# Performance work log

Measured on AMD Instinct MI355X. Metric: run time of the kernel, lower is better.

The kernel has to match this reference:

```python
import jax, jax.numpy as jnp
import numpy as np

N = 50000          # nodes
E = 1_600_000      # directed edges (before self loops)
G = 128            # graphs in batch
IN_F = 64
C1, H = 32, 4      # gat1: out_channels=32, heads=4 -> hidden 128
C2 = 64            # gat2: out_channels=64, heads=1, concat=False
OUT_F = 2
EPS = 1e-5
NEG_SLOPE = 0.2    # PyG GATv2Conv default


def setup_inputs() -> dict:
    key = jax.random.key(0)
    ks = jax.random.split(key, 24)
    s = 0.05
    inp = {
        'x': jax.random.normal(ks[0], (N, IN_F), jnp.float32),
        'edge_index': jax.random.randint(ks[1], (2, E), 0, N, dtype=jnp.int64),
        'batch': jnp.sort(jax.random.randint(ks[2], (N,), 0, G, dtype=jnp.int64)),
        # GATv2 layer 1 (in=64 -> 4 heads x 32)
        'W1l': jax.random.normal(ks[3], (IN_F, H * C1), jnp.float32) * s,
        'b1l': jnp.zeros((H * C1,), jnp.float32),
        'W1r': jax.random.normal(ks[4], (IN_F, H * C1), jnp.float32) * s,
        'b1r': jnp.zeros((H * C1,), jnp.float32),
        'att1': jax.random.normal(ks[5], (H, C1), jnp.float32) * s,
        'bias1': jnp.zeros((H * C1,), jnp.float32),
        # GATv2 layer 2 (in=128 -> 1 head x 64, no concat)
        'W2l': jax.random.normal(ks[6], (H * C1, C2), jnp.float32) * s,
        'b2l': jnp.zeros((C2,), jnp.float32),
        'W2r': jax.random.normal(ks[7], (H * C1, C2), jnp.float32) * s,
        'b2r': jnp.zeros((C2,), jnp.float32),
        'att2': jax.random.normal(ks[8], (1, C2), jnp.float32) * s,
        'bias2': jnp.zeros((C2,), jnp.float32),
        # batchnorms (batch-statistics normalization)
        'bn1_g': jnp.ones((H * C1,), jnp.float32),
        'bn1_b': jnp.zeros((H * C1,), jnp.float32),
        'bn2_g': jnp.ones((C2,), jnp.float32),
        'bn2_b': jnp.zeros((C2,), jnp.float32),
        # final linear: CL2_F*3 -> out_f
        'lin_w': jax.random.normal(ks[9], (3 * C2, OUT_F), jnp.float32) * s,
        'lin_b': jnp.zeros((OUT_F,), jnp.float32),
    }
    return inp


def _gatv2(x, Wl, bl, Wr, br, att, bias, src, dst, heads, ch, concat, n_nodes):
    # x: [N, F_in]; src/dst: [E'] (self loops already appended)
    xl = (x @ Wl + bl).reshape(n_nodes, heads, ch)  # source transform
    xr = (x @ Wr + br).reshape(n_nodes, heads, ch)  # target transform
    m = jax.nn.leaky_relu(xl[src] + xr[dst], NEG_SLOPE)      # [E', H, C]
    logits = jnp.einsum('ehc,hc->eh', m, att)                # [E', H]
    # segment softmax over destination nodes (every node has a self loop)
    mx = jax.ops.segment_max(logits, dst, num_segments=n_nodes)
    a = jnp.exp(logits - mx[dst])
    denom = jax.ops.segment_sum(a, dst, num_segments=n_nodes)
    alpha = a / denom[dst]                                   # [E', H]
    out = jax.ops.segment_sum(xl[src] * alpha[..., None], dst,
                              num_segments=n_nodes)          # [N, H, C]
    if concat:
        out = out.reshape(n_nodes, heads * ch)
    else:
        out = out.mean(axis=1)
    return out + bias


def _bn(h, gamma, beta):
    mu = h.mean(axis=0)
    var = h.var(axis=0)
    return (h - mu) * jax.lax.rsqrt(var + EPS) * gamma + beta


def reference(x, edge_index, batch, W1l, b1l, W1r, b1r, att1, bias1,
              W2l, b2l, W2r, b2r, att2, bias2,
              bn1_g, bn1_b, bn2_g, bn2_b, lin_w, lin_b):
    n = x.shape[0]
    loops = jnp.arange(n, dtype=edge_index.dtype)
    src = jnp.concatenate([edge_index[0], loops])  # PyG add_self_loops=True
    dst = jnp.concatenate([edge_index[1], loops])

    h = jax.nn.relu(_gatv2(x, W1l, b1l, W1r, b1r, att1, bias1,
                           src, dst, H, C1, True, n))
    h = _bn(h, bn1_g, bn1_b)      # dropout is identity (eval)
    h = jax.nn.relu(_gatv2(h, W2l, b2l, W2r, b2r, att2, bias2,
                           src, dst, 1, C2, False, n))
    h = _bn(h, bn2_g, bn2_b)

    x0 = jax.ops.segment_sum(h, batch, num_segments=G)                  # add pool
    cnt = jax.ops.segment_sum(jnp.ones((n, 1), h.dtype), batch, num_segments=G)
    x1 = x0 / jnp.maximum(cnt, 1.0)                                     # mean pool
    x2 = jax.ops.segment_max(h, batch, num_segments=G)                  # max pool
    feat = jnp.concatenate([x0, x1, x2], axis=-1)                       # [G, 3*C2]
    return feat @ lin_w + lin_b
```

## Files before the change

### kernel.cpp

```cpp
#include <hip/hip_runtime.h>
#include <hip/hip_fp16.h>
#include <math.h>

#define BSHIFT 7
#define CHUNK  8192
#define CAP    6144

__device__ inline __half2 habs2_(__half2 x){
  union { __half2 h; unsigned u; } c; c.h = x; c.u &= 0x7FFF7FFFu; return c.h;
}
__device__ inline __half2 lrelu2_(__half2 x, __half2 c06, __half2 c04){
  return __hfma2(c04, habs2_(x), __hmul2(c06, x));
}

__global__ __launch_bounds__(256) void k_pre(const int* __restrict__ ei, int E, int N, int NB,
    int* __restrict__ bfill, unsigned* __restrict__ ebuf,
    const float* __restrict__ X,
    const float* __restrict__ Wl, const float* __restrict__ bl,
    const float* __restrict__ Wr, const float* __restrict__ br,
    __half* __restrict__ outl, __half* __restrict__ outr, int bb){
  __shared__ float xs[32][64];
  if ((int)blockIdx.x < bb){
    int* hist = (int*)&xs[0][0];
    int base = blockIdx.x*CHUNK;
    int EL = E + N;
    int end = min(base + CHUNK, EL);
    for (int i = threadIdx.x; i < NB; i += 256) hist[i] = 0;
    __syncthreads();
    for (int e = base + threadIdx.x; e < end; e += 256){
      int d = (e < E) ? ei[E + e] : (e - E);
      atomicAdd(&hist[d >> BSHIFT], 1);
    }
    __syncthreads();
    for (int b = threadIdx.x; b < NB; b += 256){
      int c = hist[b];
      hist[b] = (c > 0) ? (b*CAP + atomicAdd(&bfill[b], c)) : 0;
    }
    __syncthreads();
    for (int e = base + threadIdx.x; e < end; e += 256){
      int s, d;
      if (e < E){ s = ei[e]; d = ei[E + e]; } else { s = d = e - E; }
      int pos = atomicAdd(&hist[d >> BSHIFT], 1);
      ebuf[pos] = (unsigned)s | ((unsigned)d << 16);
    }
  } else {
    const int tid = threadIdx.x;
    const int n0 = ((int)blockIdx.x - bb)*32;
    for (int t = tid; t < 32*64; t += 256){
      int r = t >> 6, c = t & 63;
      int node = n0 + r;
      xs[r][c] = (node < N) ? X[(size_t)node*64 + c] : 0.f;
    }
    __syncthreads();
    const int jg = tid & 63;
    const int ng = tid >> 6;
    const int q  = jg*4;
    const bool isL = (q < 128);
    const float* W = isL ? Wl : Wr;
    const int jj   = isL ? q : q - 128;
    const float* bbp = isL ? bl : br;
    __half* OUT    = isL ? outl : outr;
    const float4 bias4 = *(const float4*)(bbp + jj);
    float acc[8][4];
    #pragma unroll
    for (int n = 0; n < 8; ++n){ acc[n][0]=acc[n][1]=acc[n][2]=acc[n][3]=0.f; }
    for (int k = 0; k < 64; k += 4){
      const float4 w0 = *(const float4*)(W + (size_t)(k+0)*128 + jj);
      const float4 w1 = *(const float4*)(W + (size_t)(k+1)*128 + jj);
      const float4 w2 = *(const float4*)(W + (size_t)(k+2)*128 + jj);
      const float4 w3 = *(const float4*)(W + (size_t)(k+3)*128 + jj);
      #pragma unroll
      for (int n = 0; n < 8; ++n){
        const float4 xv = *(const float4*)(&xs[ng*8 + n][k]);
        acc[n][0] = fmaf(xv.w,w3.x, fmaf(xv.z,w2.x, fmaf(xv.y,w1.x, fmaf(xv.x,w0.x, acc[n][0]))));
        acc[n][1] = fmaf(xv.w,w3.y, fmaf(xv.z,w2.y, fmaf(xv.y,w1.y, fmaf(xv.x,w0.y, acc[n][1]))));
        acc[n][2] = fmaf(xv.w,w3.z, fmaf(xv.z,w2.z, fmaf(xv.y,w1.z, fmaf(xv.x,w0.z, acc[n][2]))));
        acc[n][3] = fmaf(xv.w,w3.w, fmaf(xv.z,w2.w, fmaf(xv.y,w1.w, fmaf(xv.x,w0.w, acc[n][3]))));
      }
    }
    #pragma unroll
    for (int n = 0; n < 8; ++n){
      int node = n0 + ng*8 + n;
      if (node < N){
        union { __half2 h[2]; uint2 u; } cv;
        cv.h[0] = __floats2half2_rn(acc[n][0]+bias4.x, acc[n][1]+bias4.y);
        cv.h[1] = __floats2half2_rn(acc[n][2]+bias4.z, acc[n][3]+bias4.w);
        *(uint2*)(OUT + (size_t)node*128 + jj) = cv.u;
      }
    }
  }
}

__global__ __launch_bounds__(1024) void k_fine(const unsigned* __restrict__ ebuf,
    const int* __restrict__ bfill, int N, int NB,
    int* __restrict__ rstart, int* __restrict__ rend, int* __restrict__ esrc){
  __shared__ int cnt[128];
  __shared__ int sc[128];
  __shared__ int base[128];
  int b = blockIdx.x;
  int n0 = b << BSHIFT;
  int nn = min(128, N - n0);
  int e0 = b*CAP;
  int e1 = e0 + bfill[b];
  if (threadIdx.x < 128) cnt[threadIdx.x] = 0;
  __syncthreads();
  for (int e = e0 + threadIdx.x; e < e1; e += 1024)
    atomicAdd(&cnt[(ebuf[e] >> 16) & 127], 1);
  __syncthreads();
  if (threadIdx.x < 128) sc[threadIdx.x] = cnt[threadIdx.x];
  __syncthreads();
  for (int off = 1; off < 128; off <<= 1){
    int v = 0;
    if (threadIdx.x < 128 && (int)threadIdx.x >= off) v = sc[threadIdx.x - off];
    __syncthreads();
    if (threadIdx.x < 128) sc[threadIdx.x] += v;
    __syncthreads();
  }
  if (threadIdx.x < 128){
    int bs = e0 + sc[threadIdx.x] - cnt[threadIdx.x];
    base[threadIdx.x] = bs;
    if ((int)threadIdx.x < nn){
      rstart[n0 + threadIdx.x] = bs;
      rend[n0 + threadIdx.x]   = bs + cnt[threadIdx.x];
    }
    cnt[threadIdx.x] = 0;
  }
  __syncthreads();
  for (int e = e0 + threadIdx.x; e < e1; e += 1024){
    unsigned pk = ebuf[e];
    int local = (int)(pk >> 16) & 127;
    int pos = base[local] + atomicAdd(&cnt[local], 1);
    esrc[pos] = (int)(pk & 0xffffu);
  }
}

__global__ __launch_bounds__(256) void k_dhist(const int* __restrict__ rstart, const int* __restrict__ rend,
                                               int N, int* __restrict__ dh){
  __shared__ int h[512];
  for (int i = threadIdx.x; i < 512; i += 256) h[i] = 0;
  __syncthreads();
  #pragma unroll
  for (int k = 0; k < 4; ++k){
    int n = blockIdx.x*1024 + k*256 + threadIdx.x;
    if (n < N){
      int deg = rend[n] - rstart[n];
      atomicAdd(&h[511 - min(deg, 511)], 1);
    }
  }
  __syncthreads();
  for (int i = threadIdx.x; i < 512; i += 256){
    int c = h[i];
    if (c) atomicAdd(&dh[i], c);
  }
}

__global__ __launch_bounds__(512) void k_dscan(const int* __restrict__ dh, int* __restrict__ dfill){
  __shared__ int s[512];
  int tid = threadIdx.x;
  int v = dh[tid];
  s[tid] = v; __syncthreads();
  for (int off = 1; off < 512; off <<= 1){
    int t = (tid >= off) ? s[tid - off] : 0;
    __syncthreads();
    s[tid] += t;
    __syncthreads();
  }
  dfill[tid] = s[tid] - v;
}

__global__ __launch_bounds__(256) void k_dperm(const int* __restrict__ rstart, const int* __restrict__ rend,
                                               int N, int* __restrict__ dfill, int* __restrict__ perm){
  __shared__ int h[512];
  __shared__ int mybin[1024];
  int base_n = blockIdx.x*1024;
  for (int i = threadIdx.x; i < 512; i += 256) h[i] = 0;
  __syncthreads();
  #pragma unroll
  for (int k = 0; k < 4; ++k){
    int n = base_n + k*256 + threadIdx.x;
    if (n < N){
      int deg = rend[n] - rstart[n];
      int b = 511 - min(deg, 511);
      mybin[k*256 + threadIdx.x] = b;
      atomicAdd(&h[b], 1);
    }
  }
  __syncthreads();
  for (int i = threadIdx.x; i < 512; i += 256){
    int c = h[i];
    h[i] = c ? atomicAdd(&dfill[i], c) : 0;
  }
  __syncthreads();
  #pragma unroll
  for (int k = 0; k < 4; ++k){
    int n = base_n + k*256 + threadIdx.x;
    if (n < N){
      int pos = atomicAdd(&h[mybin[k*256 + threadIdx.x]], 1);
      perm[pos] = n;
    }
  }
}

__global__ __launch_bounds__(256) void k_gemm2(const __half2* __restrict__ X2,
    const float* __restrict__ Wl, const float* __restrict__ bl,
    const float* __restrict__ Wr, const float* __restrict__ br,
    __half* __restrict__ outl, __half* __restrict__ outr, int N,
    const float* __restrict__ bsum, const float* __restrict__ bsq,
    const float* __restrict__ gam, const float* __restrict__ bet){
  __shared__ float xs[32][128];
  const int tid = threadIdx.x;
  const int n0 = blockIdx.x*32;
  const float invN = 1.f/(float)N;
  for (int t = tid; t < 32*64; t += 256){
    int r = t >> 6, c2 = t & 63, c = c2*2;
    int node = n0 + r;
    float2 v = (node < N) ? __half22float2(X2[(size_t)node*64 + c2]) : make_float2(0.f,0.f);
    float m0 = bsum[c]*invN,   m1 = bsum[c+1]*invN;
    float r0 = rsqrtf(bsq[c]*invN   - m0*m0 + 1e-5f);
    float r1 = rsqrtf(bsq[c+1]*invN - m1*m1 + 1e-5f);
    v.x = (v.x - m0) * r0 * gam[c  ] + bet[c  ];
    v.y = (v.y - m1) * r1 * gam[c+1] + bet[c+1];
    xs[r][c] = v.x; xs[r][c+1] = v.y;
  }
  __syncthreads();
  const int jg = tid & 31;
  const int ng = tid >> 5;
  const int q  = jg*4;
  const bool isL = (q < 64);
  const float* W = isL ? Wl : Wr;
  const int jj   = isL ? q : q - 64;
  const float* bbp = isL ? bl : br;
  __half* OUT    = isL ? outl : outr;
  const float4 bias4 = *(const float4*)(bbp + jj);
  float acc[4][4];
  #pragma unroll
  for (int n = 0; n < 4; ++n){ acc[n][0]=acc[n][1]=acc[n][2]=acc[n][3]=0.f; }
  for (int k = 0; k < 128; k += 4){
    const float4 w0 = *(const float4*)(W + (size_t)(k+0)*64 + jj);
    const float4 w1 = *(const float4*)(W + (size_t)(k+1)*64 + jj);
    const float4 w2 = *(const float4*)(W + (size_t)(k+2)*64 + jj);
    const float4 w3 = *(const float4*)(W + (size_t)(k+3)*64 + jj);
    #pragma unroll
    for (int n = 0; n < 4; ++n){
      const float4 xv = *(const float4*)(&xs[ng*4 + n][k]);
      acc[n][0] = fmaf(xv.w,w3.x, fmaf(xv.z,w2.x, fmaf(xv.y,w1.x, fmaf(xv.x,w0.x, acc[n][0]))));
      acc[n][1] = fmaf(xv.w,w3.y, fmaf(xv.z,w2.y, fmaf(xv.y,w1.y, fmaf(xv.x,w0.y, acc[n][1]))));
      acc[n][2] = fmaf(xv.w,w3.z, fmaf(xv.z,w2.z, fmaf(xv.y,w1.z, fmaf(xv.x,w0.z, acc[n][2]))));
      acc[n][3] = fmaf(xv.w,w3.w, fmaf(xv.z,w2.w, fmaf(xv.y,w1.w, fmaf(xv.x,w0.w, acc[n][3]))));
    }
  }
  #pragma unroll
  for (int n = 0; n < 4; ++n){
    int node = n0 + ng*4 + n;
    if (node < N){
      union { __half2 h[2]; uint2 u; } cv;
      cv.h[0] = __floats2half2_rn(acc[n][0]+bias4.x, acc[n][1]+bias4.y);
      cv.h[1] = __floats2half2_rn(acc[n][2]+bias4.z, acc[n][3]+bias4.w);
      *(uint2*)(OUT + (size_t)node*64 + jj) = cv.u;
    }
  }
}

__global__ __launch_bounds__(256, 6) void k_gat1(const __half* __restrict__ xl, const __half* __restrict__ xr,
    const int* __restrict__ rstart, const int* __restrict__ rend,
    const int* __restrict__ esrc, const int* __restrict__ perm,
    const float* __restrict__ att, const float* __restrict__ bias,
    __half* __restrict__ h1, int N){
  int wv = (blockIdx.x*256 + threadIdx.x) >> 6;
  int lane = threadIdx.x & 63;
  int g = lane >> 4;
  int t = lane & 15;
  int idx = wv*4 + g;
  bool live = idx < N;
  int nd = perm[min(idx, N-1)];
  int c0 = t*8;
  const __half2 c06 = __float2half2_rn(0.6f);
  const __half2 c04 = __float2half2_rn(0.4f);
  union { uint4 u; __half2 h[4]; } xru;
  xru.u = *(const uint4*)(xr + (size_t)nd*128 + c0);
  float4 a0 = *(const float4*)(att + c0);
  float4 a1 = *(const float4*)(att + c0 + 4);
  __half2 av2[4] = { __floats2half2_rn(a0.x,a0.y), __floats2half2_rn(a0.z,a0.w),
                     __floats2half2_rn(a1.x,a1.y), __floats2half2_rn(a1.z,a1.w) };
  int r0 = rstart[nd];
  int r1 = rend[nd];
  int d  = r1 - r0;
  d = max(d, __shfl_xor(d, 16));
  d = max(d, __shfl_xor(d, 32));
  const char* xb = (const char*)xl;
  const unsigned cb = (unsigned)(c0*2);
  float s = 0.f;
  __half2 acc2[4];
  #pragma unroll
  for (int k = 0; k < 4; ++k) acc2[k] = __float2half2_rn(0.f);
  union V { uint4 u; __half2 h[4]; } cur[4], nxt[4];
  #pragma unroll
  for (int q = 0; q < 4; ++q){
    unsigned j = (unsigned)esrc[r0 + q] & 0xFFFFu;
    cur[q].u = *(const uint4*)(xb + ((j << 8) + cb));
  }
  for (int i = 0; i < d; i += 4){
    #pragma unroll
    for (int q = 0; q < 4; ++q){
      unsigned j = (unsigned)esrc[r0 + i + 4 + q] & 0xFFFFu;
      nxt[q].u = *(const uint4*)(xb + ((j << 8) + cb));
    }
    #pragma unroll
    for (int q = 0; q < 4; ++q){
      bool valid = (r0 + i + q) < r1;
      __half2 p2 = __float2half2_rn(0.f);
      #pragma unroll
      for (int k = 0; k < 4; ++k){
        __half2 m2 = __hadd2(cur[q].h[k], xru.h[k]);
        p2 = __hfma2(lrelu2_(m2, c06, c04), av2[k], p2);
      }
      float p = __low2float(p2) + __high2float(p2);
      p += __shfl_xor(p, 1);
      p += __shfl_xor(p, 2);
      float w = valid ? __expf(p) : 0.f;
      s += w;
      __half2 w2 = __float2half2_rn(w);
      #pragma unroll
      for (int k = 0; k < 4; ++k) acc2[k] = __hfma2(w2, cur[q].h[k], acc2[k]);
    }
    #pragma unroll
    for (int q = 0; q < 4; ++q) cur[q] = nxt[q];
  }
  if (live){
    float inv = 1.f/s;
    float4 b0 = *(const float4*)(bias + c0);
    float4 b1 = *(const float4*)(bias + c0 + 4);
    float bv[8] = {b0.x,b0.y,b0.z,b0.w,b1.x,b1.y,b1.z,b1.w};
    union { __half2 h[4]; uint4 u; } o;
    #pragma unroll
    for (int k = 0; k < 4; ++k){
      float2 af = __half22float2(acc2[k]);
      float f0 = fmaxf(af.x*inv + bv[2*k],   0.f);
      float f1 = fmaxf(af.y*inv + bv[2*k+1], 0.f);
      o.h[k] = __floats2half2_rn(f0, f1);
    }
    *(uint4*)(h1 + (size_t)nd*128 + c0) = o.u;
  }
}

__global__ __launch_bounds__(256, 6) void k_gat2(const __half* __restrict__ xl, const __half* __restrict__ xr,
    const int* __restrict__ rstart, const int* __restrict__ rend,
    const int* __restrict__ esrc, const int* __restrict__ perm,
    const float* __restrict__ att, const float* __restrict__ bias,
    __half* __restrict__ h2, int N){
  int wv = (blockIdx.x*256 + threadIdx.x) >> 6;
  int lane = threadIdx.x & 63;
  int g = lane >> 3;
  int t = lane & 7;
  int idx = wv*8 + g;
  bool live = idx < N;
  int nd = perm[min(idx, N-1)];
  int c0 = t*8;
  const __half2 c06 = __float2half2_rn(0.6f);
  const __half2 c04 = __float2half2_rn(0.4f);
  union { uint4 u; __half2 h[4]; } xru;
  xru.u = *(const uint4*)(xr + (size_t)nd*64 + c0);
  float4 a0 = *(const float4*)(att + c0);
  float4 a1 = *(const float4*)(att + c0 + 4);
  __half2 av2[4] = { __floats2half2_rn(a0.x,a0.y), __floats2half2_rn(a0.z,a0.w),
                     __floats2half2_rn(a1.x,a1.y), __floats2half2_rn(a1.z,a1.w) };
  int r0 = rstart[nd];
  int r1 = rend[nd];
  int d  = r1 - r0;
  d = max(d, __shfl_xor(d, 8));
  d = max(d, __shfl_xor(d, 16));
  d = max(d, __shfl_xor(d, 32));
  const char* xb = (const char*)xl;
  const unsigned cb = (unsigned)(c0*2);
  float s = 0.f;
  __half2 acc2[4];
  #pragma unroll
  for (int k = 0; k < 4; ++k) acc2[k] = __float2half2_rn(0.f);
  union V { uint4 u; __half2 h[4]; } cur[4], nxt[4];
  #pragma unroll
  for (int q = 0; q < 4; ++q){
    unsigned j = (unsigned)esrc[r0 + q] & 0xFFFFu;
    cur[q].u = *(const uint4*)(xb + ((j << 7) + cb));
  }
  for (int i = 0; i < d; i += 4){
    #pragma unroll
    for (int q = 0; q < 4; ++q){
      unsigned j = (unsigned)esrc[r0 + i + 4 + q] & 0xFFFFu;
      nxt[q].u = *(const uint4*)(xb + ((j << 7) + cb));
    }
    #pragma unroll
    for (int q = 0; q < 4; ++q){
      bool valid = (r0 + i + q) < r1;
      __half2 p2 = __float2half2_rn(0.f);
      #pragma unroll
      for (int k = 0; k < 4; ++k){
        __half2 m2 = __hadd2(cur[q].h[k], xru.h[k]);
        p2 = __hfma2(lrelu2_(m2, c06, c04), av2[k], p2);
      }
      float p = __low2float(p2) + __high2float(p2);
      p += __shfl_xor(p, 1);
      p += __shfl_xor(p, 2);
      p += __shfl_xor(p, 4);
      float w = valid ? __expf(p) : 0.f;
      s += w;
      __half2 w2 = __float2half2_rn(w);
      #pragma unroll
      for (int k = 0; k < 4; ++k) acc2[k] = __hfma2(w2, cur[q].h[k], acc2[k]);
    }
    #pragma unroll
    for (int q = 0; q < 4; ++q) cur[q] = nxt[q];
  }
  if (live){
    float inv = 1.f/s;
    float4 b0 = *(const float4*)(bias + c0);
    float4 b1 = *(const float4*)(bias + c0 + 4);
    float bv[8] = {b0.x,b0.y,b0.z,b0.w,b1.x,b1.y,b1.z,b1.w};
    union { __half2 h[4]; uint4 u; } o;
    #pragma unroll
    for (int k = 0; k < 4; ++k){
      float2 af = __half22float2(acc2[k]);
      float f0 = fmaxf(af.x*inv + bv[2*k],   0.f);
      float f1 = fmaxf(af.y*inv + bv[2*k+1], 0.f);
      o.h[k] = __floats2half2_rn(f0, f1);
    }
    *(uint4*)(h2 + (size_t)nd*64 + c0) = o.u;
  }
}

template<int C>
__global__ __launch_bounds__(256) void k_bnstats(const __half* __restrict__ h, int N,
    float* __restrict__ sum, float* __restrict__ sq){
  constexpr int RPB = 256/C;
  int c = threadIdx.x % C;
  int sub = threadIdx.x / C;
  float s = 0.f, q = 0.f;
  for (int r = blockIdx.x*RPB + sub; r < N; r += gridDim.x*RPB){
    float v = __half2float(h[(size_t)r*C + c]);
    s += v; q += v*v;
  }
  __shared__ float ls[256], lq[256];
  ls[threadIdx.x] = s; lq[threadIdx.x] = q;
  __syncthreads();
  if (threadIdx.x < C){
    float S = ls[c], Q = lq[c];
    #pragma unroll
    for (int u = 1; u < RPB; ++u){ S += ls[u*C + c]; Q += lq[u*C + c]; }
    atomicAdd(&sum[c], S);
    atomicAdd(&sq[c], Q);
  }
}

__global__ __launch_bounds__(256) void k_pool(const __half* __restrict__ h2, const int* __restrict__ batch, int N,
    const float* __restrict__ bsum, const float* __restrict__ bsq,
    const float* __restrict__ g, const float* __restrict__ b,
    const float* __restrict__ lw, const float* __restrict__ lb,
    float* __restrict__ out){
  int gr = blockIdx.x;
  int lo = 0, hi = N;
  while (lo < hi){ int mid = (lo+hi)>>1; if (batch[mid] < gr) lo = mid+1; else hi = mid; }
  int r0 = lo;
  lo = r0; hi = N;
  while (lo < hi){ int mid = (lo+hi)>>1; if (batch[mid] < gr+1) lo = mid+1; else hi = mid; }
  int r1 = lo;
  int c = threadIdx.x & 63;
  int sub = threadIdx.x >> 6;
  const float invN = 1.f/(float)N;
  float m = bsum[c]*invN;
  float rs = rsqrtf(bsq[c]*invN - m*m + 1e-5f);
  float aff_s = rs*g[c];
  float aff_b = b[c] - m*aff_s;
  float s = 0.f, mx = -INFINITY;
  for (int r = r0 + sub; r < r1; r += 4){
    float v = __half2float(h2[(size_t)r*64 + c])*aff_s + aff_b;
    s += v; mx = fmaxf(mx, v);
  }
  __shared__ float ls[256], lm[256], ft[192];
  ls[threadIdx.x] = s; lm[threadIdx.x] = mx;
  __syncthreads();
  if (threadIdx.x < 64){
    float S = ls[c] + ls[64+c] + ls[128+c] + ls[192+c];
    float M = fmaxf(fmaxf(lm[c], lm[64+c]), fmaxf(lm[128+c], lm[192+c]));
    float cnt = (float)max(r1 - r0, 1);
    ft[c]       = S;
    ft[64 + c]  = S/cnt;
    ft[128 + c] = M;
  }
  __syncthreads();
  if (threadIdx.x < 2){
    float acc = lb[threadIdx.x];
    #pragma unroll 4
    for (int k = 0; k < 192; ++k) acc += ft[k] * lw[k*2 + threadIdx.x];
    out[gr*2 + threadIdx.x] = acc;
  }
}

extern "C" void kernel_launch(void* const* d_in, const int* in_sizes, int n_in,
                              void* d_out, int out_size, void* d_ws, size_t ws_size,
                              hipStream_t stream) {
  const float* x    = (const float*)d_in[0];
  const int*   ei   = (const int*)d_in[1];
  const int*   batch= (const int*)d_in[2];
  const float* W1l  = (const float*)d_in[3];
  const float* b1l  = (const float*)d_in[4];
  const float* W1r  = (const float*)d_in[5];
  const float* b1r  = (const float*)d_in[6];
  const float* att1 = (const float*)d_in[7];
  const float* bias1= (const float*)d_in[8];
  const float* W2l  = (const float*)d_in[9];
  const float* b2l  = (const float*)d_in[10];
  const float* W2r  = (const float*)d_in[11];
  const float* b2r  = (const float*)d_in[12];
  const float* att2 = (const float*)d_in[13];
  const float* bias2= (const float*)d_in[14];
  const float* g1   = (const float*)d_in[15];
  const float* be1  = (const float*)d_in[16];
  const float* g2   = (const float*)d_in[17];
  const float* be2  = (const float*)d_in[18];
  const float* lw   = (const float*)d_in[19];
  const float* lb   = (const float*)d_in[20];

  const int N  = in_sizes[0] / 64;
  const int E  = in_sizes[1] / 2;
  const int EL = E + N;
  const int G  = 128;
  const int NB = (N + 127) >> BSHIFT;

  char* p = (char*)d_ws;
  auto carve = [&](size_t bytes)->char*{ char* r = p; p += (bytes + 255) & ~(size_t)255; return r; };
  int* zero   = (int*)carve((size_t)(NB + 512 + 384)*4);
  int* bfill  = zero;
  int* dh     = zero + NB;
  float* stats = (float*)(zero + NB + 512);
  float* bn1_sum = stats;
  float* bn1_sq  = stats + 128;
  float* bn2_sum = stats + 256;
  float* bn2_sq  = stats + 320;
  int* dfill  = (int*)carve((size_t)512*4);
  int* rstart = (int*)carve((size_t)N*4);
  int* rend   = (int*)carve((size_t)N*4);
  int* perm   = (int*)carve((size_t)N*4);
  unsigned* ebuf = (unsigned*)carve((size_t)NB*CAP*4);
  int* esrc   = (int*)carve((size_t)(NB*CAP + 1024)*4);
  __half* xl1 = (__half*)carve((size_t)N*128*2);
  __half* xr1 = (__half*)carve((size_t)N*128*2);
  __half* h1  = (__half*)carve((size_t)N*128*2);
  __half* xl2 = xl1;
  __half* xr2 = xl1 + (size_t)N*64;
  __half* h2  = xr1;

  hipMemsetAsync(zero, 0, (size_t)(NB + 512 + 384)*4, stream);

  const int bb = (EL + CHUNK - 1)/CHUNK;
  const int gb = (N + 31)/32;
  const int db = (N + 1023)/1024;
  k_pre<<<bb + gb, 256, 0, stream>>>(ei, E, N, NB, bfill, ebuf,
                                     x, W1l, b1l, W1r, b1r, xl1, xr1, bb);
  k_fine<<<NB, 1024, 0, stream>>>(ebuf, bfill, N, NB, rstart, rend, esrc);
  k_dhist<<<db, 256, 0, stream>>>(rstart, rend, N, dh);
  k_dscan<<<1, 512, 0, stream>>>(dh, dfill);
  k_dperm<<<db, 256, 0, stream>>>(rstart, rend, N, dfill, perm);

  const int nb1 = ((N + 3)/4*64 + 255)/256;
  const int nb2 = ((N + 7)/8*64 + 255)/256;
  k_gat1<<<nb1, 256, 0, stream>>>(xl1, xr1, rstart, rend, esrc, perm, att1, bias1, h1, N);
  k_bnstats<128><<<256, 256, 0, stream>>>(h1, N, bn1_sum, bn1_sq);
  k_gemm2<<<gb, 256, 0, stream>>>((const __half2*)h1, W2l, b2l, W2r, b2r, xl2, xr2, N,
                                  bn1_sum, bn1_sq, g1, be1);
  k_gat2<<<nb2, 256, 0, stream>>>(xl2, xr2, rstart, rend, esrc, perm, att2, bias2, h2, N);
  k_bnstats<64><<<256, 256, 0, stream>>>(h2, N, bn2_sum, bn2_sq);
  k_pool<<<G, 256, 0, stream>>>(h2, batch, N, bn2_sum, bn2_sq, g2, be2, lw, lb, (float*)d_out);
}
```

Baseline: 369.4 us.

## Fuse degree histogram into k_fine and BN statistics into GAT kernels

Removes the separate degree-histogram kernel by having k_fine atomically add each node's in-degree bin to the global histogram. Removes both BN-statistics kernels by accumulating per-channel sum and sum-of-squares in shared memory inside k_gat1/k_gat2, then flushing them to global with atomics. This saves three launches and two extra reads of h1/h2. In exchange it adds shared-memory float atomics and barriers to the GAT kernels, global atomic contention in k_fine, and it sums BN statistics from fp32 values rather than from the fp16-rounded outputs.

New measurement: 591.2 us. 60.0% more time.

```diff
diff --git a/kernel.cpp b/kernel.cpp
--- a/kernel.cpp
+++ b/kernel.cpp
@@ -93,7 +93,8 @@
 
 __global__ __launch_bounds__(1024) void k_fine(const unsigned* __restrict__ ebuf,
     const int* __restrict__ bfill, int N, int NB,
-    int* __restrict__ rstart, int* __restrict__ rend, int* __restrict__ esrc){
+    int* __restrict__ rstart, int* __restrict__ rend, int* __restrict__ esrc,
+    int* __restrict__ dh){
   __shared__ int cnt[128];
   __shared__ int sc[128];
   __shared__ int base[128];
@@ -122,6 +123,7 @@
     if ((int)threadIdx.x < nn){
       rstart[n0 + threadIdx.x] = bs;
       rend[n0 + threadIdx.x]   = bs + cnt[threadIdx.x];
+      atomicAdd(&dh[511 - min(cnt[threadIdx.x], 511)], 1);
     }
     cnt[threadIdx.x] = 0;
   }
@@ -131,26 +133,6 @@
     int local = (int)(pk >> 16) & 127;
     int pos = base[local] + atomicAdd(&cnt[local], 1);
     esrc[pos] = (int)(pk & 0xffffu);
-  }
-}
-
-__global__ __launch_bounds__(256) void k_dhist(const int* __restrict__ rstart, const int* __restrict__ rend,
-                                               int N, int* __restrict__ dh){
-  __shared__ int h[512];
-  for (int i = threadIdx.x; i < 512; i += 256) h[i] = 0;
-  __syncthreads();
-  #pragma unroll
-  for (int k = 0; k < 4; ++k){
-    int n = blockIdx.x*1024 + k*256 + threadIdx.x;
-    if (n < N){
-      int deg = rend[n] - rstart[n];
-      atomicAdd(&h[511 - min(deg, 511)], 1);
-    }
-  }
-  __syncthreads();
-  for (int i = threadIdx.x; i < 512; i += 256){
-    int c = h[i];
-    if (c) atomicAdd(&dh[i], c);
   }
 }
 
@@ -265,7 +247,11 @@
     const int* __restrict__ rstart, const int* __restrict__ rend,
     const int* __restrict__ esrc, const int* __restrict__ perm,
     const float* __restrict__ att, const float* __restrict__ bias,
-    __half* __restrict__ h1, int N){
+    __half* __restrict__ h1, int N,
+    float* __restrict__ bn_sum, float* __restrict__ bn_sq){
+  __shared__ float bs[128], bq[128];
+  if (threadIdx.x < 128){ bs[threadIdx.x] = 0.f; bq[threadIdx.x] = 0.f; }
+  __syncthreads();
   int wv = (blockIdx.x*256 + threadIdx.x) >> 6;
   int lane = threadIdx.x & 63;
   int g = lane >> 4;
@@ -334,12 +320,20 @@
     union { __half2 h[4]; uint4 u; } o;
     #pragma unroll
     for (int k = 0; k < 4; ++k){
-      float2 af = __half22float2(acc2[k]);
-      float f0 = fmaxf(af.x*inv + bv[2*k],   0.f);
-      float f1 = fmaxf(af.y*inv + bv[2*k+1], 0.f);
+      float f0 = fmaxf(__low2float(acc2[k])*inv  + bv[2*k],   0.f);
+      float f1 = fmaxf(__high2float(acc2[k])*inv + bv[2*k+1], 0.f);
       o.h[k] = __floats2half2_rn(f0, f1);
+      atomicAdd(&bs[c0 + 2*k],     f0);
+      atomicAdd(&bs[c0 + 2*k + 1], f1);
+      atomicAdd(&bq[c0 + 2*k],     f0*f0);
+      atomicAdd(&bq[c0 + 2*k + 1], f1*f1);
     }
     *(uint4*)(h1 + (size_t)nd*128 + c0) = o.u;
+  }
+  __syncthreads();
+  if (threadIdx.x < 128){
+    atomicAdd(&bn_sum[threadIdx.x], bs[threadIdx.x]);
+    atomicAdd(&bn_sq[threadIdx.x],  bq[threadIdx.x]);
   }
 }
 
@@ -347,7 +341,11 @@
     const int* __restrict__ rstart, const int* __restrict__ rend,
     const int* __restrict__ esrc, const int* __restrict__ perm,
     const float* __restrict__ att, const float* __restrict__ bias,
-    __half* __restrict__ h2, int N){
+    __half* __restrict__ h2, int N,
+    float* __restrict__ bn_sum, float* __restrict__ bn_sq){
+  __shared__ float bs[64], bq[64];
+  if (threadIdx.x < 64){ bs[threadIdx.x] = 0.f; bq[threadIdx.x] = 0.f; }
+  __syncthreads();
   int wv = (blockIdx.x*256 + threadIdx.x) >> 6;
   int lane = threadIdx.x & 63;
   int g = lane >> 3;
@@ -418,35 +416,20 @@
     union { __half2 h[4]; uint4 u; } o;
     #pragma unroll
     for (int k = 0; k < 4; ++k){
-      float2 af = __half22float2(acc2[k]);
-      float f0 = fmaxf(af.x*inv + bv[2*k],   0.f);
-      float f1 = fmaxf(af.y*inv + bv[2*k+1], 0.f);
+      float f0 = fmaxf(__low2float(acc2[k])*inv  + bv[2*k],   0.f);
+      float f1 = fmaxf(__high2float(acc2[k])*inv + bv[2*k+1], 0.f);
       o.h[k] = __floats2half2_rn(f0, f1);
+      atomicAdd(&bs[c0 + 2*k],     f0);
+      atomicAdd(&bs[c0 + 2*k + 1], f1);
+      atomicAdd(&bq[c0 + 2*k],     f0*f0);
+      atomicAdd(&bq[c0 + 2*k + 1], f1*f1);
     }
     *(uint4*)(h2 + (size_t)nd*64 + c0) = o.u;
   }
-}
-
-template<int C>
-__global__ __launch_bounds__(256) void k_bnstats(const __half* __restrict__ h, int N,
-    float* __restrict__ sum, float* __restrict__ sq){
-  constexpr int RPB = 256/C;
-  int c = threadIdx.x % C;
-  int sub = threadIdx.x / C;
-  float s = 0.f, q = 0.f;
-  for (int r = blockIdx.x*RPB + sub; r < N; r += gridDim.x*RPB){
-    float v = __half2float(h[(size_t)r*C + c]);
-    s += v; q += v*v;
-  }
-  __shared__ float ls[256], lq[256];
-  ls[threadIdx.x] = s; lq[threadIdx.x] = q;
-  __syncthreads();
-  if (threadIdx.x < C){
-    float S = ls[c], Q = lq[c];
-    #pragma unroll
-    for (int u = 1; u < RPB; ++u){ S += ls[u*C + c]; Q += lq[u*C + c]; }
-    atomicAdd(&sum[c], S);
-    atomicAdd(&sq[c], Q);
+  __syncthreads();
+  if (threadIdx.x < 64){
+    atomicAdd(&bn_sum[threadIdx.x], bs[threadIdx.x]);
+    atomicAdd(&bn_sq[threadIdx.x],  bq[threadIdx.x]);
   }
 }
 
@@ -555,18 +538,17 @@
   const int db = (N + 1023)/1024;
   k_pre<<<bb + gb, 256, 0, stream>>>(ei, E, N, NB, bfill, ebuf,
                                      x, W1l, b1l, W1r, b1r, xl1, xr1, bb);
-  k_fine<<<NB, 1024, 0, stream>>>(ebuf, bfill, N, NB, rstart, rend, esrc);
-  k_dhist<<<db, 256, 0, stream>>>(rstart, rend, N, dh);
+  k_fine<<<NB, 1024, 0, stream>>>(ebuf, bfill, N, NB, rstart, rend, esrc, dh);
   k_dscan<<<1, 512, 0, stream>>>(dh, dfill);
   k_dperm<<<db, 256, 0, stream>>>(rstart, rend, N, dfill, perm);
 
   const int nb1 = ((N + 3)/4*64 + 255)/256;
   const int nb2 = ((N + 7)/8*64 + 255)/256;
-  k_gat1<<<nb1, 256, 0, stream>>>(xl1, xr1, rstart, rend, esrc, perm, att1, bias1, h1, N);
-  k_bnstats<128><<<256, 256, 0, stream>>>(h1, N, bn1_sum, bn1_sq);
+  k_gat1<<<nb1, 256, 0, stream>>>(xl1, xr1, rstart, rend, esrc, perm, att1, bias1, h1, N,
+                                  bn1_sum, bn1_sq);
   k_gemm2<<<gb, 256, 0, stream>>>((const __half2*)h1, W2l, b2l, W2r, b2r, xl2, xr2, N,
                                   bn1_sum, bn1_sq, g1, be1);
-  k_gat2<<<nb2, 256, 0, stream>>>(xl2, xr2, rstart, rend, esrc, perm, att2, bias2, h2, N);
-  k_bnstats<64><<<256, 256, 0, stream>>>(h2, N, bn2_sum, bn2_sq);
+  k_gat2<<<nb2, 256, 0, stream>>>(xl2, xr2, rstart, rend, esrc, perm, att2, bias2, h2, N,
+                                  bn2_sum, bn2_sq);
   k_pool<<<G, 256, 0, stream>>>(h2, batch, N, bn2_sum, bn2_sq, g2, be2, lw, lb, (float*)d_out);
 }
```
